# Kernel optimization log

Measured on AMD Instinct MI355X. Metric: run time of the kernel, lower is better.

## Reference

```python
import jax, jax.numpy as jnp
import numpy as np

N_START, N_TO, E, H = 100000, 50000, 1000000, 128

def setup_inputs() -> dict:
    key = jax.random.key(0)
    ks = jax.random.split(key, 8)
    return {
        "z_start": jax.random.normal(ks[0], (N_START, H), dtype=jnp.float32),
        "z_to": jax.random.normal(ks[1], (N_TO, H), dtype=jnp.float32),
        "row": jax.random.randint(ks[2], (E,), 0, N_START, dtype=jnp.int64),
        "col": jax.random.randint(ks[3], (E,), 0, N_TO, dtype=jnp.int64),
        "W1": jax.random.normal(ks[4], (2 * H, H), dtype=jnp.float32) * (1.0 / np.sqrt(2 * H)),
        "b1": jnp.zeros((H,), dtype=jnp.float32),
        "W2": jax.random.normal(ks[5], (H, 1), dtype=jnp.float32) * (1.0 / np.sqrt(H)),
        "b2": jnp.zeros((1,), dtype=jnp.float32),
    }

def reference(z_start, z_to, row, col, W1, b1, W2, b2):
    # gather node embeddings by edge endpoints, concat along feature dim
    z = jnp.concatenate([z_start[row], z_to[col]], axis=-1)  # [E, 2H]
    h = jax.nn.relu(z @ W1 + b1)                              # [E, H]
    out = h @ W2 + b2                                         # [E, 1]
    return out.reshape(-1)
```

## Files before the change

kernel.cpp:

```cpp
#include <hip/hip_runtime.h>
#include <hip/hip_bf16.h>
#include <stdint.h>

typedef unsigned short u16;
typedef __attribute__((ext_vector_type(8))) short short8;
typedef __attribute__((ext_vector_type(4))) float float4v;

__device__ __forceinline__ u16 f2bf(float x) {
    union { float f; unsigned int u; } v; v.f = x;
    unsigned int r = v.u + 0x7fffu + ((v.u >> 16) & 1u);
    return (u16)(r >> 16);
}

__device__ __forceinline__ void ld_g2l16(const void* g, void* l) {
    __builtin_amdgcn_global_load_lds(
        (const __attribute__((address_space(1))) void*)g,
        (__attribute__((address_space(3))) void*)l, 16, 0, 0);
}

__device__ __forceinline__ float sbyte_f(int w, int j) {
    return (float)((w << (24 - 8 * j)) >> 24);
}

__global__ __launch_bounds__(256) void w1_pack(
    const float* __restrict__ W1, u16* __restrict__ w1p)
{
    int w = blockIdx.x * 256 + threadIdx.x;
    int lanep = w & 63, t = (w >> 6) & 7, kc = w >> 9;
    short8 o;
#pragma unroll
    for (int j = 0; j < 8; ++j) {
        int k = kc * 32 + (lanep >> 4) * 8 + j;
        int n = t * 16 + (lanep & 15);
        o[j] = (short)f2bf(W1[k * 128 + n]);
    }
    *(short8*)(w1p + (size_t)w * 8) = o;
}

__global__ __launch_bounds__(256) void uv_gemm(
    const float* __restrict__ zs, const float* __restrict__ zt,
    const u16* __restrict__ w1p, const float* __restrict__ b1,
    char* __restrict__ U8, char* __restrict__ V8,
    float* __restrict__ su, float* __restrict__ sv,
    int M1, int M2, int nU)
{
    __shared__ u16 Alds[16384];
    __shared__ u16 Blds[16384];

    const int tid = threadIdx.x, wave = tid >> 6, lane = tid & 63;
    const int m15 = lane & 15, quad = lane >> 4;
    const bool isV = (int)blockIdx.x >= nU;
    const float* zsrc = isV ? zt : zs;
    char* dst = isV ? V8 : U8;
    float* sdst = isV ? sv : su;
    const int row0 = (isV ? ((int)blockIdx.x - nU) : (int)blockIdx.x) * 128;
    const int M = isV ? M2 : M1;
    const int nrows = (M - row0) < 128 ? (M - row0) : 128;

    const u16* wsrc = w1p + (isV ? 16384 : 0);
#pragma unroll
    for (int it = 0; it < 8; ++it) {
        int off = (wave * 8 + it) * 1024;
        ld_g2l16((const char*)wsrc + off + lane * 16, (char*)Blds + off);
    }

#pragma unroll
    for (int it = 0; it < 8; ++it) {
        int r = it * 16 + wave * 4 + (lane >> 4);
        int q = lane & 15;
        int c = q ^ (r & 15);
        int rr = r < nrows ? r : (nrows - 1);
        const float4* src = (const float4*)(zsrc + (size_t)(row0 + rr) * 128 + c * 8);
        float4 x = src[0], y = src[1];
        short8 o;
        o[0] = (short)f2bf(x.x); o[1] = (short)f2bf(x.y);
        o[2] = (short)f2bf(x.z); o[3] = (short)f2bf(x.w);
        o[4] = (short)f2bf(y.x); o[5] = (short)f2bf(y.y);
        o[6] = (short)f2bf(y.z); o[7] = (short)f2bf(y.w);
        *(short8*)((char*)Alds + r * 256 + q * 16) = o;
    }

    __builtin_amdgcn_s_waitcnt(0);
    __syncthreads();

    float4v acc[2][8];
#pragma unroll
    for (int a = 0; a < 2; ++a)
#pragma unroll
        for (int b = 0; b < 8; ++b)
            acc[a][b] = (float4v){0.f, 0.f, 0.f, 0.f};

#pragma unroll
    for (int kc = 0; kc < 4; ++kc) {
        short8 Af[2];
#pragma unroll
        for (int mtl = 0; mtl < 2; ++mtl) {
            int r = wave * 32 + mtl * 16 + m15;
            int c = kc * 4 + quad;
            int q = c ^ (r & 15);
            Af[mtl] = *(const short8*)((const char*)Alds + r * 256 + q * 16);
        }
#pragma unroll
        for (int t = 0; t < 8; ++t) {
            short8 Bf = *(const short8*)((const char*)Blds + (kc * 8 + t) * 1024 + lane * 16);
#pragma unroll
            for (int mtl = 0; mtl < 2; ++mtl)
                acc[mtl][t] = __builtin_amdgcn_mfma_f32_16x16x32_bf16(
                    Af[mtl], Bf, acc[mtl][t], 0, 0, 0);
        }
    }

    float b1v[8];
#pragma unroll
    for (int t = 0; t < 8; ++t) b1v[t] = isV ? 0.f : b1[t * 16 + m15];

#pragma unroll
    for (int mtl = 0; mtl < 2; ++mtl) {
#pragma unroll
        for (int r = 0; r < 4; ++r) {
            const int rr = wave * 32 + mtl * 16 + quad * 4 + r;
            float vals[8];
            float vmax = 0.f;
#pragma unroll
            for (int t = 0; t < 8; ++t) {
                float x = acc[mtl][t][r] + b1v[t];
                vals[t] = x;
                vmax = fmaxf(vmax, fabsf(x));
            }
            vmax = fmaxf(vmax, __shfl_xor(vmax, 1));
            vmax = fmaxf(vmax, __shfl_xor(vmax, 2));
            vmax = fmaxf(vmax, __shfl_xor(vmax, 4));
            vmax = fmaxf(vmax, __shfl_xor(vmax, 8));
            const float scl = vmax * (1.f / 127.f);
            const float rs = vmax > 0.f ? 127.f / vmax : 0.f;
            if (rr < nrows) {
                if (m15 == 0) sdst[row0 + rr] = scl;
#pragma unroll
                for (int t = 0; t < 8; ++t) {
                    int q = __float2int_rn(vals[t] * rs);
                    q = q > 127 ? 127 : (q < -127 ? -127 : q);
                    dst[(size_t)(row0 + rr) * 128 + t * 16 + m15] = (char)q;
                }
            }
        }
    }
}

__global__ __launch_bounds__(256) void edge_out(
    const char* __restrict__ U8, const char* __restrict__ V8,
    const float* __restrict__ su, const float* __restrict__ sv,
    const int* __restrict__ row, const int* __restrict__ col,
    const float* __restrict__ W2, const float* __restrict__ b2,
    float* __restrict__ out, int E)
{
    const int tid = threadIdx.x, m15 = tid & 15, g = tid >> 4;
    float w2f[8];
#pragma unroll
    for (int j = 0; j < 8; ++j) w2f[j] = W2[m15 * 8 + j];
    const float b2v = b2[0];
    const int e0 = blockIdx.x * 128;

    int re[8], ce[8];
#pragma unroll
    for (int it = 0; it < 8; ++it) {
        int e = e0 + it * 16 + g;
        int ec = e < E ? e : E - 1;
        re[it] = row[ec];
        ce[it] = col[ec];
    }
    __builtin_amdgcn_sched_barrier(0);

    uint2 qu[8], qv[8];
    float fsu[8], fsv[8];
#pragma unroll
    for (int it = 0; it < 8; ++it) {
        qu[it] = *(const uint2*)(U8 + (size_t)(unsigned)re[it] * 128 + m15 * 8);
        qv[it] = *(const uint2*)(V8 + (size_t)(unsigned)ce[it] * 128 + m15 * 8);
        fsu[it] = su[re[it]];
        fsv[it] = sv[ce[it]];
    }
    __builtin_amdgcn_sched_barrier(0);

#pragma unroll
    for (int it = 0; it < 8; ++it) {
        const float a = fsu[it], b = fsv[it];
        const int u0 = (int)qu[it].x, u1 = (int)qu[it].y;
        const int v0 = (int)qv[it].x, v1 = (int)qv[it].y;
        float s = 0.f;
#pragma unroll
        for (int j = 0; j < 4; ++j) {
            float h0 = fmaf(a, sbyte_f(u0, j), b * sbyte_f(v0, j));
            h0 = fmaxf(h0, 0.f);
            s = fmaf(h0, w2f[j], s);
            float h1 = fmaf(a, sbyte_f(u1, j), b * sbyte_f(v1, j));
            h1 = fmaxf(h1, 0.f);
            s = fmaf(h1, w2f[4 + j], s);
        }
        s += __shfl_xor(s, 1);
        s += __shfl_xor(s, 2);
        s += __shfl_xor(s, 4);
        s += __shfl_xor(s, 8);
        int e = e0 + it * 16 + g;
        if (m15 == 0 && e < E) out[e] = s + b2v;
    }
}

__global__ __launch_bounds__(256) void edge_mlp_naive(
    const float* __restrict__ zs, const float* __restrict__ zt,
    const int* __restrict__ row, const int* __restrict__ col,
    const float* __restrict__ W1, const float* __restrict__ b1,
    const float* __restrict__ W2, const float* __restrict__ b2,
    float* __restrict__ out, int E)
{
    __shared__ float zr[4][256];
    int wave = threadIdx.x >> 6, lane = threadIdx.x & 63;
    int e = blockIdx.x * 4 + wave;
    int ec = e < E ? e : E - 1;
    const float* a = zs + (size_t)row[ec] * 128;
    const float* bb = zt + (size_t)col[ec] * 128;
    zr[wave][lane] = a[lane];
    zr[wave][64 + lane] = a[64 + lane];
    zr[wave][128 + lane] = bb[lane];
    zr[wave][192 + lane] = bb[64 + lane];
    __syncthreads();
    float h0 = b1[lane], h1 = b1[64 + lane];
    for (int k = 0; k < 256; ++k) {
        float zk = zr[wave][k];
        h0 = fmaf(zk, W1[k * 128 + lane], h0);
        h1 = fmaf(zk, W1[k * 128 + 64 + lane], h1);
    }
    h0 = h0 > 0.f ? h0 : 0.f;
    h1 = h1 > 0.f ? h1 : 0.f;
    float s = fmaf(h0, W2[lane], h1 * W2[64 + lane]);
    for (int m = 1; m < 64; m <<= 1) s += __shfl_xor(s, m);
    if (lane == 0 && e < E) out[e] = s + b2[0];
}

extern "C" void kernel_launch(void* const* d_in, const int* in_sizes, int n_in,
                              void* d_out, int out_size, void* d_ws, size_t ws_size,
                              hipStream_t stream) {
    const float* zs = (const float*)d_in[0];
    const float* zt = (const float*)d_in[1];
    const int*  row = (const int*)d_in[2];
    const int*  col = (const int*)d_in[3];
    const float* W1 = (const float*)d_in[4];
    const float* b1 = (const float*)d_in[5];
    const float* W2 = (const float*)d_in[6];
    const float* b2 = (const float*)d_in[7];
    float* out = (float*)d_out;

    const int nzs = in_sizes[0];
    const int nzt = in_sizes[1];
    const int E   = in_sizes[2];
    const int M1  = nzs / 128;
    const int M2  = nzt / 128;

    const size_t need = (size_t)(M1 + M2) * 4 + 65536 + (size_t)nzs + (size_t)nzt;
    if (ws_size < need) {
        int nb = (E + 3) / 4;
        edge_mlp_naive<<<nb, 256, 0, stream>>>(zs, zt, row, col, W1, b1, W2, b2, out, E);
        return;
    }

    float* su = (float*)d_ws;
    float* sv = su + M1;
    u16* w1p  = (u16*)(sv + M2);
    char* U8  = (char*)(w1p + 32768);
    char* V8  = U8 + (size_t)nzs;

    w1_pack<<<16, 256, 0, stream>>>(W1, w1p);

    const int nU = (M1 + 127) / 128;
    const int nV = (M2 + 127) / 128;
    uv_gemm<<<nU + nV, 256, 0, stream>>>(zs, zt, w1p, b1, U8, V8, su, sv, M1, M2, nU);

    edge_out<<<(E + 127) / 128, 256, 0, stream>>>(U8, V8, su, sv, row, col, W2, b2, out, E);
}
```

Before: 189.8 us.

## Bin edges by source-row range before gathering to improve cache locality

Adds an edge_bin kernel that groups edges into 8 buckets by source-row range. Each edge is packed as a 64-bit (row, col, edge id) tuple, with atomic cursors handing out slots per bucket. edge_out then walks the buckets, so each stretch of work touches a narrower slice of U8, meant to raise L2/MALL hit rates on the random gathers. The cost is an extra pass over row/col, an 8-byte tuple write and read per edge, atomics, and scattered output writes. Edges that overflow a bucket fall back to a slow scalar path.

```diff
diff --git a/kernel.cpp b/kernel.cpp
--- a/kernel.cpp
+++ b/kernel.cpp
@@ -3,6 +3,7 @@
 #include <stdint.h>
 
 typedef unsigned short u16;
+typedef unsigned long long u64;
 typedef __attribute__((ext_vector_type(8))) short short8;
 typedef __attribute__((ext_vector_type(4))) float float4v;
 
@@ -23,8 +24,9 @@
 }
 
 __global__ __launch_bounds__(256) void w1_pack(
-    const float* __restrict__ W1, u16* __restrict__ w1p)
-{
+    const float* __restrict__ W1, u16* __restrict__ w1p, int* __restrict__ cursor)
+{
+    if (blockIdx.x == 0 && threadIdx.x < 8) cursor[threadIdx.x] = 0;
     int w = blockIdx.x * 256 + threadIdx.x;
     int lanep = w & 63, t = (w >> 6) & 7, kc = w >> 9;
     short8 o;
@@ -146,62 +148,124 @@
     }
 }
 
+__global__ __launch_bounds__(256) void edge_bin(
+    const int* __restrict__ row, const int* __restrict__ col,
+    u64* __restrict__ tup, int* __restrict__ cursor,
+    int E, float binv, int C,
+    const char* __restrict__ U8, const char* __restrict__ V8,
+    const float* __restrict__ su, const float* __restrict__ sv,
+    const float* __restrict__ W2, const float* __restrict__ b2,
+    float* __restrict__ out)
+{
+    __shared__ int lcnt[8];
+    __shared__ int lbase[8];
+    const int tid = threadIdx.x;
+    if (tid < 8) lcnt[tid] = 0;
+    __syncthreads();
+    const int eb = blockIdx.x * 4096;
+    int rr[16], cc[16], bb[16], rk[16];
+#pragma unroll
+    for (int it = 0; it < 16; ++it) {
+        int e = eb + it * 256 + tid;
+        rk[it] = -1;
+        if (e < E) {
+            int r = row[e], c = col[e];
+            int b = (int)((float)r * binv);
+            b = b > 7 ? 7 : b;
+            rr[it] = r; cc[it] = c; bb[it] = b;
+            rk[it] = atomicAdd(&lcnt[b], 1);
+        }
+    }
+    __syncthreads();
+    if (tid < 8) lbase[tid] = atomicAdd(&cursor[tid], lcnt[tid]);
+    __syncthreads();
+#pragma unroll
+    for (int it = 0; it < 16; ++it) {
+        if (rk[it] < 0) continue;
+        int e = eb + it * 256 + tid;
+        int slot = lbase[bb[it]] + rk[it];
+        if (slot < C) {
+            tup[(size_t)bb[it] * C + slot] =
+                (u64)(unsigned)rr[it] | ((u64)(unsigned)cc[it] << 17) | ((u64)(unsigned)e << 34);
+        } else {
+            float a = su[rr[it]], bs = sv[cc[it]];
+            const signed char* up = (const signed char*)(U8 + (size_t)rr[it] * 128);
+            const signed char* vp = (const signed char*)(V8 + (size_t)cc[it] * 128);
+            float s = 0.f;
+            for (int j = 0; j < 128; ++j) {
+                float h = fmaf(a, (float)up[j], bs * (float)vp[j]);
+                h = fmaxf(h, 0.f);
+                s = fmaf(h, W2[j], s);
+            }
+            out[e] = s + b2[0];
+        }
+    }
+}
+
 __global__ __launch_bounds__(256) void edge_out(
     const char* __restrict__ U8, const char* __restrict__ V8,
     const float* __restrict__ su, const float* __restrict__ sv,
-    const int* __restrict__ row, const int* __restrict__ col,
+    const u64* __restrict__ tup, const int* __restrict__ cursor,
     const float* __restrict__ W2, const float* __restrict__ b2,
-    float* __restrict__ out, int E)
+    float* __restrict__ out, int C, int chunks_per_bin)
 {
     const int tid = threadIdx.x, m15 = tid & 15, g = tid >> 4;
+    const int bin = (int)blockIdx.x & 7;
+    int chunk = (int)blockIdx.x >> 3;
+    int cnt = cursor[bin];
+    cnt = cnt < C ? cnt : C;
     float w2f[8];
 #pragma unroll
     for (int j = 0; j < 8; ++j) w2f[j] = W2[m15 * 8 + j];
     const float b2v = b2[0];
-    const int e0 = blockIdx.x * 128;
-
-    int re[8], ce[8];
-#pragma unroll
-    for (int it = 0; it < 8; ++it) {
-        int e = e0 + it * 16 + g;
-        int ec = e < E ? e : E - 1;
-        re[it] = row[ec];
-        ce[it] = col[ec];
-    }
-    __builtin_amdgcn_sched_barrier(0);
-
-    uint2 qu[8], qv[8];
-    float fsu[8], fsv[8];
-#pragma unroll
-    for (int it = 0; it < 8; ++it) {
-        qu[it] = *(const uint2*)(U8 + (size_t)(unsigned)re[it] * 128 + m15 * 8);
-        qv[it] = *(const uint2*)(V8 + (size_t)(unsigned)ce[it] * 128 + m15 * 8);
-        fsu[it] = su[re[it]];
-        fsv[it] = sv[ce[it]];
-    }
-    __builtin_amdgcn_sched_barrier(0);
-
-#pragma unroll
-    for (int it = 0; it < 8; ++it) {
-        const float a = fsu[it], b = fsv[it];
-        const int u0 = (int)qu[it].x, u1 = (int)qu[it].y;
-        const int v0 = (int)qv[it].x, v1 = (int)qv[it].y;
-        float s = 0.f;
-#pragma unroll
-        for (int j = 0; j < 4; ++j) {
-            float h0 = fmaf(a, sbyte_f(u0, j), b * sbyte_f(v0, j));
-            h0 = fmaxf(h0, 0.f);
-            s = fmaf(h0, w2f[j], s);
-            float h1 = fmaf(a, sbyte_f(u1, j), b * sbyte_f(v1, j));
-            h1 = fmaxf(h1, 0.f);
-            s = fmaf(h1, w2f[4 + j], s);
-        }
-        s += __shfl_xor(s, 1);
-        s += __shfl_xor(s, 2);
-        s += __shfl_xor(s, 4);
-        s += __shfl_xor(s, 8);
-        int e = e0 + it * 16 + g;
-        if (m15 == 0 && e < E) out[e] = s + b2v;
+    const u64* tb = tup + (size_t)bin * C;
+
+    for (; chunk * 128 < cnt; chunk += chunks_per_bin) {
+        const int base = chunk * 128;
+
+        u64 t[8];
+#pragma unroll
+        for (int it = 0; it < 8; ++it) {
+            int idx = base + it * 16 + g;
+            t[it] = tb[idx < cnt ? idx : cnt - 1];
+        }
+        __builtin_amdgcn_sched_barrier(0);
+
+        uint2 qu[8], qv[8];
+        float fsu[8], fsv[8];
+#pragma unroll
+        for (int it = 0; it < 8; ++it) {
+            int r = (int)(t[it] & 0x1FFFF);
+            int c = (int)((t[it] >> 17) & 0x1FFFF);
+            qu[it] = *(const uint2*)(U8 + (size_t)(unsigned)r * 128 + m15 * 8);
+            qv[it] = *(const uint2*)(V8 + (size_t)(unsigned)c * 128 + m15 * 8);
+            fsu[it] = su[r];
+            fsv[it] = sv[c];
+        }
+        __builtin_amdgcn_sched_barrier(0);
+
+#pragma unroll
+        for (int it = 0; it < 8; ++it) {
+            const float a = fsu[it], b = fsv[it];
+            const int u0 = (int)qu[it].x, u1 = (int)qu[it].y;
+            const int v0 = (int)qv[it].x, v1 = (int)qv[it].y;
+            float s = 0.f;
+#pragma unroll
+            for (int j = 0; j < 4; ++j) {
+                float h0 = fmaf(a, sbyte_f(u0, j), b * sbyte_f(v0, j));
+                h0 = fmaxf(h0, 0.f);
+                s = fmaf(h0, w2f[j], s);
+                float h1 = fmaf(a, sbyte_f(u1, j), b * sbyte_f(v1, j));
+                h1 = fmaxf(h1, 0.f);
+                s = fmaf(h1, w2f[4 + j], s);
+            }
+            s += __shfl_xor(s, 1);
+            s += __shfl_xor(s, 2);
+            s += __shfl_xor(s, 4);
+            s += __shfl_xor(s, 8);
+            int idx = base + it * 16 + g;
+            if (m15 == 0 && idx < cnt) out[(int)(t[it] >> 34)] = s + b2v;
+        }
     }
 }
 
@@ -255,24 +319,39 @@
     const int M1  = nzs / 128;
     const int M2  = nzt / 128;
 
-    const size_t need = (size_t)(M1 + M2) * 4 + 65536 + (size_t)nzs + (size_t)nzt;
-    if (ws_size < need) {
+    int C = 65536;
+    while (C < E / 4 + 1024) C <<= 1;
+
+    const size_t tup_b = (size_t)8 * C * 8;
+    const size_t need = tup_b + 64 + (size_t)M1 * 4 + (size_t)M2 * 4 + 65536
+                      + (size_t)nzs + (size_t)nzt;
+    const bool shapes_ok = (M1 <= 131072) && (M2 <= 131072) && (E > 0) && (E < (1 << 30));
+
+    if (!shapes_ok || ws_size < need) {
         int nb = (E + 3) / 4;
         edge_mlp_naive<<<nb, 256, 0, stream>>>(zs, zt, row, col, W1, b1, W2, b2, out, E);
         return;
     }
 
-    float* su = (float*)d_ws;
-    float* sv = su + M1;
-    u16* w1p  = (u16*)(sv + M2);
-    char* U8  = (char*)(w1p + 32768);
-    char* V8  = U8 + (size_t)nzs;
-
-    w1_pack<<<16, 256, 0, stream>>>(W1, w1p);
+    u64* tup    = (u64*)d_ws;
+    int* cursor = (int*)((char*)d_ws + tup_b);
+    float* su   = (float*)((char*)cursor + 64);
+    float* sv   = su + M1;
+    u16* w1p    = (u16*)(sv + M2);
+    char* U8    = (char*)(w1p + 32768);
+    char* V8    = U8 + (size_t)nzs;
+
+    w1_pack<<<16, 256, 0, stream>>>(W1, w1p, cursor);
 
     const int nU = (M1 + 127) / 128;
     const int nV = (M2 + 127) / 128;
     uv_gemm<<<nU + nV, 256, 0, stream>>>(zs, zt, w1p, b1, U8, V8, su, sv, M1, M2, nU);
 
-    edge_out<<<(E + 127) / 128, 256, 0, stream>>>(U8, V8, su, sv, row, col, W2, b2, out, E);
-}
+    const int rpb = (M1 + 7) / 8;
+    const float binv = 1.0f / (float)rpb;
+    edge_bin<<<(E + 4095) / 4096, 256, 0, stream>>>(
+        row, col, tup, cursor, E, binv, C, U8, V8, su, sv, W2, b2, out);
+
+    const int cpb = 1024;
+    edge_out<<<8 * cpb, 256, 0, stream>>>(U8, V8, su, sv, tup, cursor, W2, b2, out, C, cpb);
+}
```

Result: faster. 179.5 us (-5.5%).
